# Kernel tuning notes

Hardware: AMD Instinct MI355X
Metric: run time of the kernel (lower is better)

Reference implementation:

```python
import jax, jax.numpy as jnp
import numpy as np

D = 768       # model dim
H = 12        # num heads
DH = 64       # hidden_dim per head (D == H*DH)
DT = 32       # time_dim
KTEMP = 1.0   # k_temperature
LN_EPS = 1e-5


def setup_inputs() -> dict:
    key = jax.random.key(0)
    ks = jax.random.split(key, 10)
    B, T = 2, 2048
    states = jax.random.normal(ks[0], (B, T, D), jnp.float32)
    attention_mask = jnp.ones((B, T), jnp.int32)
    s = 0.02
    Wq = jax.random.normal(ks[1], (H * DH, D), jnp.float32) * s
    Wk = jax.random.normal(ks[2], (H * DH, D), jnp.float32) * s
    bk = jax.random.normal(ks[3], (H * DH,), jnp.float32) * s
    Wv = jax.random.normal(ks[4], (H * DH, D), jnp.float32) * s
    bv = jnp.zeros((H * DH,), jnp.float32)           # V.bias zeroed in __init__
    Wo = jax.random.normal(ks[5], (D, H * DH), jnp.float32) * s
    bo = jnp.zeros((D,), jnp.float32)                # O.bias zeroed in __init__
    q_bias = jnp.zeros((H * DH,), jnp.float32)
    time_angle = jax.random.uniform(ks[6], (H, DT), jnp.float32) ** 10 + 1e-8
    head_time_delta = jax.random.uniform(ks[7], (H,), jnp.float32)
    ln_gamma = jnp.ones((D,), jnp.float32)
    ln_beta = jnp.zeros((D,), jnp.float32)
    return {"states": states, "attention_mask": attention_mask,
            "Wq": Wq, "Wk": Wk, "bk": bk, "Wv": Wv, "bv": bv,
            "Wo": Wo, "bo": bo, "q_bias": q_bias,
            "time_angle": time_angle, "head_time_delta": head_time_delta,
            "ln_gamma": ln_gamma, "ln_beta": ln_beta}


def reference(states, attention_mask, Wq, Wk, bk, Wv, bv, Wo, bo, q_bias,
              time_angle, head_time_delta, ln_gamma, ln_beta):
    B, T, _ = states.shape
    dtype = states.dtype
    mask = attention_mask.astype(dtype)[..., None, None]  # B T 1 1

    inv_sqrt_dh = 1.0 / np.sqrt(DH).astype(np.float32)

    def get_time(delta):
        # delta: [1,H,1] or scalar 0.0
        pos = jnp.arange(T, dtype=dtype)[:, None, None]     # T 1 1
        ang = (pos + delta) * time_angle[None]              # T H Dt
        c, s = jnp.cos(ang), jnp.sin(ang)
        return jnp.concatenate([c + s, c - s], axis=-1) * inv_sqrt_dh  # T H 2Dt

    # --- q path ---
    q = states @ Wq.T - jnp.exp(q_bias)                     # B T (H*Dh), Q has no bias
    q = jax.nn.sigmoid(q.reshape(B, T, H, DH)) / DH * mask  # B T H Dh
    time_q = get_time(head_time_delta[None, :, None])       # T H 2Dt (with delta)
    time_k = get_time(0.0)                                  # T H 2Dt
    q_timed = q.sum(-1, keepdims=True) * time_q             # B T H 2Dt
    # scores: B T(query) L(key) H -- the large materialized tensor
    scores = jnp.einsum('bthd,lhd->btlh', q_timed, time_k)

    # --- kv path ---
    k = (states @ Wk.T + bk).reshape(B, T, H, DH) / KTEMP * mask
    v = (states @ Wv.T + bv).reshape(B, T, H, DH)
    kv = jax.nn.softmax(k, axis=-1) * v                     # B T H Dh

    # --- aggregate ---
    loading = jnp.einsum('btlh,blhd->bthd', scores, kv).reshape(B, T, D)
    attn_out = loading @ Wo.T + bo

    # residual + layernorm (dropout is identity in eval)
    x = states + attn_out
    mu = x.mean(-1, keepdims=True)
    var = x.var(-1, keepdims=True)
    return (x - mu) * jax.lax.rsqrt(var + LN_EPS) * ln_gamma + ln_beta
```

## Files before the change

### kernel.cpp

```cpp
#include <hip/hip_runtime.h>
#include <math.h>
#include <stdint.h>

#define TT 2048
#define BB 2
#define DD 768
#define HH 12
#define DHH 64
#define DTT 32
#define NROW 4096

typedef float v4 __attribute__((ext_vector_type(4)));
typedef __attribute__((ext_vector_type(8))) short s8v;
typedef __attribute__((ext_vector_type(4))) float f4v;
typedef unsigned short u16;
typedef __attribute__((ext_vector_type(4))) unsigned short us4;

__device__ __forceinline__ u16 f2bf(float x) {
  unsigned u = __builtin_bit_cast(unsigned, x);
  u += 0x7fffu + ((u >> 16) & 1u);
  return (u16)(u >> 16);
}
__device__ __forceinline__ float bf2f(u16 b) {
  return __builtin_bit_cast(float, (unsigned)b << 16);
}
__device__ __forceinline__ float wave_sum(float v) {
#pragma unroll
  for (int m = 32; m > 0; m >>= 1) v += __shfl_xor(v, m, 64);
  return v;
}
__device__ __forceinline__ void gload16(const void* g, void* l) {
  __builtin_amdgcn_global_load_lds(
      (const __attribute__((address_space(1))) unsigned int*)g,
      (__attribute__((address_space(3))) unsigned int*)l, 16, 0, 0);
}
__device__ __forceinline__ void wait_vm3() {
  asm volatile("s_waitcnt vmcnt(3)" ::: "memory");
  __builtin_amdgcn_sched_barrier(0);
}
__device__ __forceinline__ void wait_vm0() {
  asm volatile("s_waitcnt vmcnt(0)" ::: "memory");
  __builtin_amdgcn_sched_barrier(0);
}
__device__ __forceinline__ void raw_barrier() {
  asm volatile("s_barrier" ::: "memory");
}

__global__ __launch_bounds__(256) void prep(
    const float* __restrict__ tang, const float* __restrict__ hdelta,
    const float* __restrict__ s, const float* __restrict__ wq,
    const float* __restrict__ wk, const float* __restrict__ wv,
    const float* __restrict__ wo, u16* __restrict__ timeqb,
    u16* __restrict__ timekb, u16* __restrict__ sb, u16* __restrict__ wqb,
    u16* __restrict__ wkvb, u16* __restrict__ wob) {
  int bid = blockIdx.x;
  if (bid < 3072) {
    int idx = bid * 256 + threadIdx.x;
    int d = idx % DTT;
    int h = (idx / DTT) % HH;
    int t = idx / (DTT * HH);
    float ang = tang[h * DTT + d];
    float sk, ck, sq, cq;
    sincosf((float)t * ang, &sk, &ck);
    sincosf(((float)t + hdelta[h]) * ang, &sq, &cq);
    timekb[t * DD + h * DHH + d]       = f2bf((ck + sk) * 0.125f);
    timekb[t * DD + h * DHH + d + DTT] = f2bf((ck - sk) * 0.125f);
    timeqb[t * DD + h * DHH + d]       = f2bf((cq + sq) * 0.125f);
    timeqb[t * DD + h * DHH + d + DTT] = f2bf((cq - sq) * 0.125f);
    return;
  }
  int idx = (bid - 3072) * 256 + threadIdx.x;
  int off = idx * 4;
  const float* src;
  u16* dst;
  int so, dof;
  if (off < 3145728) {
    src = s; dst = sb; so = off; dof = off;
  } else if (off < 3735552) {
    src = wq; dst = wqb; so = off - 3145728; dof = so;
  } else if (off < 4325376) {
    src = wk; so = off - 3735552;
    int j = so / 768, c = so - j * 768;
    int h = j >> 6, r = j & 63;
    dst = wkvb; dof = (h * 128 + r) * 768 + c;
  } else if (off < 4915200) {
    src = wv; so = off - 4325376;
    int j = so / 768, c = so - j * 768;
    int h = j >> 6, r = j & 63;
    dst = wkvb; dof = (h * 128 + 64 + r) * 768 + c;
  } else {
    src = wo; dst = wob; so = off - 4915200; dof = so;
  }
  v4 f = *(const v4*)&src[so];
  us4 o;
#pragma unroll
  for (int j = 0; j < 4; ++j) o[j] = f2bf(f[j]);
  *(us4*)&dst[dof] = o;
}

__global__ __launch_bounds__(256) void gemm_qkv_fused(
    const u16* __restrict__ A, const u16* __restrict__ Wqb,
    const u16* __restrict__ Wkvb, const float* __restrict__ qb,
    const float* __restrict__ bk, const float* __restrict__ bv,
    const int* __restrict__ amask, float* __restrict__ qsum,
    u16* __restrict__ kvb) {
  __shared__ __align__(16) u16 As[2][2176];
  __shared__ __align__(16) u16 Bs[2][4096];
  const int tid = threadIdx.x;
  const int l = tid & 63;
  const int w = tid >> 6;
  const int wr = w >> 1, wc = w & 1;
  const int bx = blockIdx.x;
  const bool isQ = bx < 6;
  const int i0 = blockIdx.y * 64;
  const u16* Bbase = isQ ? (Wqb + (size_t)bx * 128 * 768)
                         : (Wkvb + (size_t)(bx - 6) * 128 * 768);
  const int srow = tid >> 2, scol = (tid & 3) * 8;
  const u16* gA0 = A + (size_t)(i0 + srow) * 768 + scol;
  const u16* gB0 = Bbase + (size_t)srow * 768 + scol;
  const u16* gB1 = gB0 + (size_t)64 * 768;
  const int lo = tid * 8;
  f4v acc[2][4];
#pragma unroll
  for (int m = 0; m < 2; ++m)
#pragma unroll
    for (int n = 0; n < 4; ++n) acc[m][n] = (f4v){0.f, 0.f, 0.f, 0.f};

#define STAGE(kt, b)                       \
  do {                                     \
    int kb_ = (kt) << 5;                   \
    gload16(gA0 + kb_, &As[b][lo]);        \
    gload16(gB0 + kb_, &Bs[b][lo]);        \
    gload16(gB1 + kb_, &Bs[b][2048 + lo]); \
  } while (0)

  STAGE(0, 0);
  STAGE(1, 1);
  const int ar = wr * 32 + (l & 15);
  const int br = wc * 64 + (l & 15);
  const int kx = (l >> 4) * 8;
  int cb = 0;
  for (int kt = 0; kt < 24; ++kt) {
    if (kt < 23) wait_vm3();
    else wait_vm0();
    raw_barrier();
    s8v af[2], bf4[4];
#pragma unroll
    for (int m = 0; m < 2; ++m)
      af[m] = *(const s8v*)&As[cb][(ar + m * 16) * 32 + kx];
#pragma unroll
    for (int n = 0; n < 4; ++n)
      bf4[n] = *(const s8v*)&Bs[cb][(br + n * 16) * 32 + kx];
#pragma unroll
    for (int m = 0; m < 2; ++m)
#pragma unroll
      for (int n = 0; n < 4; ++n)
        acc[m][n] =
            __builtin_amdgcn_mfma_f32_16x16x32_bf16(af[m], bf4[n], acc[m][n], 0, 0, 0);
    raw_barrier();
    if (kt + 2 < 24) STAGE(kt + 2, cb);
    cb ^= 1;
  }
  __syncthreads();

  const int crow = i0 + wr * 32 + (l >> 4) * 4;
  if (isQ) {
    const int head = bx * 2 + wc;
    float eqb[4];
#pragma unroll
    for (int n = 0; n < 4; ++n)
      eqb[n] = expf(qb[head * 64 + n * 16 + (l & 15)]);
#pragma unroll
    for (int m = 0; m < 2; ++m)
#pragma unroll
      for (int r = 0; r < 4; ++r) {
        float ssum = 0.f;
#pragma unroll
        for (int n = 0; n < 4; ++n)
          ssum += 1.f / (1.f + expf(-(acc[m][n][r] - eqb[n])));
#pragma unroll
        for (int mm = 8; mm > 0; mm >>= 1) ssum += __shfl_xor(ssum, mm, 64);
        int row = crow + m * 16 + r;
        if ((l & 15) == 0)
          qsum[row * HH + head] = ssum * (float)amask[row] * (1.f / 64.f);
      }
  } else {
    const int head = bx - 6;
    u16* Ps = &As[0][0];
    if (wc == 0) {
#pragma unroll
      for (int m = 0; m < 2; ++m)
#pragma unroll
        for (int r = 0; r < 4; ++r) {
          int row = crow + m * 16 + r;
          float mk = (float)amask[row];
          float kv4[4];
#pragma unroll
          for (int n = 0; n < 4; ++n)
            kv4[n] = (acc[m][n][r] + bk[head * 64 + n * 16 + (l & 15)]) * mk;
          float mx = fmaxf(fmaxf(kv4[0], kv4[1]), fmaxf(kv4[2], kv4[3]));
#pragma unroll
          for (int mm = 8; mm > 0; mm >>= 1)
            mx = fmaxf(mx, __shfl_xor(mx, mm, 64));
          float e[4], es = 0.f;
#pragma unroll
          for (int n = 0; n < 4; ++n) { e[n] = expf(kv4[n] - mx); es += e[n]; }
#pragma unroll
          for (int mm = 8; mm > 0; mm >>= 1) es += __shfl_xor(es, mm, 64);
          float inv = 1.f / es;
          int lrow = wr * 32 + (l >> 4) * 4 + m * 16 + r;
#pragma unroll
          for (int n = 0; n < 4; ++n)
            Ps[lrow * 68 + n * 16 + (l & 15)] = f2bf(e[n] * inv);
        }
    }
    __syncthreads();
    if (wc == 1) {
#pragma unroll
      for (int m = 0; m < 2; ++m)
#pragma unroll
        for (int r = 0; r < 4; ++r) {
          int row = crow + m * 16 + r;
          int lrow = wr * 32 + (l >> 4) * 4 + m * 16 + r;
#pragma unroll
          for (int n = 0; n < 4; ++n) {
            int d = n * 16 + (l & 15);
            float p = bf2f(Ps[lrow * 68 + d]);
            float vv = acc[m][n][r] + bv[head * 64 + d];
            kvb[((size_t)row * HH + head) * 64 + d] = f2bf(p * vv);
          }
        }
    }
  }
}

__global__ __launch_bounds__(256) void calc_M(
    const u16* __restrict__ timekb, const u16* __restrict__ kvb,
    float* __restrict__ Mpart) {
  int blk = blockIdx.x;
  int split = blk & 15;
  int bh = blk >> 4;
  int b = bh / HH, h = bh % HH;
  __shared__ float Tk[64][68];
  __shared__ float Kv[64][68];
  int tid = threadIdx.x;
  int tx = tid & 15, ty = tid >> 4;
  float acc[4][4] = {};
  int t0 = split * 128;
  for (int tt = 0; tt < 128; tt += 64) {
#pragma unroll
    for (int p = 0; p < 4; ++p) {
      int f = tid + 256 * p;
      int r = f >> 4, c4 = (f & 15) << 2;
      int t = t0 + tt + r;
      us4 tk = *(const us4*)&timekb[(size_t)t * DD + h * DHH + c4];
      us4 kv = *(const us4*)&kvb[((size_t)(b * TT + t) * HH + h) * 64 + c4];
#pragma unroll
      for (int j = 0; j < 4; ++j) {
        Tk[r][c4 + j] = bf2f(tk[j]);
        Kv[r][c4 + j] = bf2f(kv[j]);
      }
    }
    __syncthreads();
#pragma unroll
    for (int kk = 0; kk < 64; ++kk) {
      v4 a = *(const v4*)&Tk[kk][ty * 4];
      v4 bv4 = *(const v4*)&Kv[kk][tx * 4];
#pragma unroll
      for (int r = 0; r < 4; ++r)
#pragma unroll
        for (int c = 0; c < 4; ++c) acc[r][c] += a[r] * bv4[c];
    }
    __syncthreads();
  }
#pragma unroll
  for (int r = 0; r < 4; ++r)
#pragma unroll
    for (int c = 0; c < 4; ++c)
      Mpart[(size_t)blk * 4096 + (tx * 4 + c) * 64 + (ty * 4 + r)] = acc[r][c];
}

__global__ __launch_bounds__(256) void reduce_M(
    const float* __restrict__ Mpart, u16* __restrict__ Mtb) {
  int idx = blockIdx.x * 256 + threadIdx.x;
  int bh = idx >> 12;
  int p = idx & 4095;
  float s = 0.f;
#pragma unroll
  for (int sp = 0; sp < 16; ++sp)
    s += Mpart[(size_t)((bh << 4) + sp) * 4096 + p];
  Mtb[(size_t)bh * 4096 + p] = f2bf(s);
}

__global__ __launch_bounds__(256) void calc_loading_mfma(
    const u16* __restrict__ timeqb, const u16* __restrict__ Mtb,
    const float* __restrict__ qsum, u16* __restrict__ loading) {
  const int bh = blockIdx.y;
  const int b = bh / HH, h = bh % HH;
  const int t0 = blockIdx.x * 128;
  __shared__ __align__(16) u16 Ms[64 * 72];
  for (int p = threadIdx.x; p < 4096; p += 256)
    Ms[(p >> 6) * 72 + (p & 63)] = Mtb[(size_t)bh * 4096 + p];
  __syncthreads();
  const int l = threadIdx.x & 63, w = threadIdx.x >> 6;
  f4v acc[2][4];
#pragma unroll
  for (int m = 0; m < 2; ++m)
#pragma unroll
    for (int n = 0; n < 4; ++n) acc[m][n] = (f4v){0.f, 0.f, 0.f, 0.f};
  const int arow = t0 + w * 32 + (l & 15);
  const int dcol = l & 15;
#pragma unroll
  for (int ks = 0; ks < 2; ++ks) {
    const int k0 = ks * 32 + (l >> 4) * 8;
    s8v af[2], bf4[4];
#pragma unroll
    for (int m = 0; m < 2; ++m)
      af[m] = *(const s8v*)&timeqb[(size_t)(arow + m * 16) * DD + h * DHH + k0];
#pragma unroll
    for (int n = 0; n < 4; ++n)
      bf4[n] = *(const s8v*)&Ms[(dcol + n * 16) * 72 + k0];
#pragma unroll
    for (int m = 0; m < 2; ++m)
#pragma unroll
      for (int n = 0; n < 4; ++n)
        acc[m][n] =
            __builtin_amdgcn_mfma_f32_16x16x32_bf16(af[m], bf4[n], acc[m][n], 0, 0, 0);
  }
  const int trow = t0 + w * 32 + (l >> 4) * 4;
  float qs[2][4];
#pragma unroll
  for (int m = 0; m < 2; ++m)
#pragma unroll
    for (int r = 0; r < 4; ++r)
      qs[m][r] = qsum[(b * TT + trow + m * 16 + r) * HH + h];
#pragma unroll
  for (int m = 0; m < 2; ++m)
#pragma unroll
    for (int n = 0; n < 4; ++n)
#pragma unroll
      for (int r = 0; r < 4; ++r) {
        int i = b * TT + trow + m * 16 + r;
        loading[(size_t)i * DD + h * DHH + n * 16 + (l & 15)] =
            f2bf(qs[m][r] * acc[m][n][r]);
      }
}

__global__ __launch_bounds__(256) void gemm_out(
    const u16* __restrict__ A, const u16* __restrict__ B, float* __restrict__ C,
    const float* __restrict__ bias, const float* __restrict__ res) {
  __shared__ __align__(16) u16 As[2][2176];
  __shared__ __align__(16) u16 Bs[2][4096];
  const int tid = threadIdx.x;
  const int l = tid & 63;
  const int w = tid >> 6;
  const int wr = w >> 1, wc = w & 1;
  const int i0 = blockIdx.y * 64, j0 = blockIdx.x * 128;
  const int srow = tid >> 2, scol = (tid & 3) * 8;
  const u16* gA0 = A + (size_t)(i0 + srow) * 768 + scol;
  const u16* gB0 = B + (size_t)(j0 + srow) * 768 + scol;
  const u16* gB1 = gB0 + (size_t)64 * 768;
  const int lo = tid * 8;
  f4v acc[2][4];
#pragma unroll
  for (int m = 0; m < 2; ++m)
#pragma unroll
    for (int n = 0; n < 4; ++n) acc[m][n] = (f4v){0.f, 0.f, 0.f, 0.f};
  STAGE(0, 0);
  STAGE(1, 1);
  const int ar = wr * 32 + (l & 15);
  const int br = wc * 64 + (l & 15);
  const int kx = (l >> 4) * 8;
  int cb = 0;
  for (int kt = 0; kt < 24; ++kt) {
    if (kt < 23) wait_vm3();
    else wait_vm0();
    raw_barrier();
    s8v af[2], bf4[4];
#pragma unroll
    for (int m = 0; m < 2; ++m)
      af[m] = *(const s8v*)&As[cb][(ar + m * 16) * 32 + kx];
#pragma unroll
    for (int n = 0; n < 4; ++n)
      bf4[n] = *(const s8v*)&Bs[cb][(br + n * 16) * 32 + kx];
#pragma unroll
    for (int m = 0; m < 2; ++m)
#pragma unroll
      for (int n = 0; n < 4; ++n)
        acc[m][n] =
            __builtin_amdgcn_mfma_f32_16x16x32_bf16(af[m], bf4[n], acc[m][n], 0, 0, 0);
    raw_barrier();
    if (kt + 2 < 24) STAGE(kt + 2, cb);
    cb ^= 1;
  }
  __syncthreads();
  const int crow = i0 + wr * 32 + (l >> 4) * 4;
  const int ccol = j0 + wc * 64 + (l & 15);
#pragma unroll
  for (int m = 0; m < 2; ++m)
#pragma unroll
    for (int n = 0; n < 4; ++n) {
      int col = ccol + n * 16;
      size_t base = (size_t)(crow + m * 16) * 768 + col;
#pragma unroll
      for (int r = 0; r < 4; ++r)
        C[base + (size_t)r * 768] =
            acc[m][n][r] + bias[col] + res[base + (size_t)r * 768];
    }
}

__global__ __launch_bounds__(256) void layernorm(
    const float* __restrict__ X, const float* __restrict__ gamma,
    const float* __restrict__ beta, float* __restrict__ out) {
  int i = blockIdx.x;
  const float* x = X + (size_t)i * 768;
  float vals[3];
  float s = 0.f, s2 = 0.f;
#pragma unroll
  for (int p = 0; p < 3; ++p) {
    float v = x[threadIdx.x + 256 * p];
    vals[p] = v;
    s += v;
    s2 += v * v;
  }
  s = wave_sum(s);
  s2 = wave_sum(s2);
  __shared__ float red[8];
  int w = threadIdx.x >> 6;
  if ((threadIdx.x & 63) == 0) {
    red[w] = s;
    red[4 + w] = s2;
  }
  __syncthreads();
  float stot = red[0] + red[1] + red[2] + red[3];
  float s2tot = red[4] + red[5] + red[6] + red[7];
  float mu = stot * (1.f / 768.f);
  float var = s2tot * (1.f / 768.f) - mu * mu;
  float rs = rsqrtf(var + 1e-5f);
#pragma unroll
  for (int p = 0; p < 3; ++p) {
    int j = threadIdx.x + 256 * p;
    out[(size_t)i * 768 + j] = (vals[p] - mu) * rs * gamma[j] + beta[j];
  }
}

extern "C" void kernel_launch(void* const* d_in, const int* in_sizes, int n_in,
                              void* d_out, int out_size, void* d_ws,
                              size_t ws_size, hipStream_t stream) {
  const float* states = (const float*)d_in[0];
  const int* amask    = (const int*)d_in[1];
  const float* Wq     = (const float*)d_in[2];
  const float* Wk     = (const float*)d_in[3];
  const float* bk     = (const float*)d_in[4];
  const float* Wv     = (const float*)d_in[5];
  const float* bv     = (const float*)d_in[6];
  const float* Wo     = (const float*)d_in[7];
  const float* bo     = (const float*)d_in[8];
  const float* qb     = (const float*)d_in[9];
  const float* tang   = (const float*)d_in[10];
  const float* hdelta = (const float*)d_in[11];
  const float* gamma  = (const float*)d_in[12];
  const float* beta   = (const float*)d_in[13];
  float* out = (float*)d_out;
  float* ws = (float*)d_ws;

  u16* timeqb = (u16*)(ws + 0);
  u16* timekb = (u16*)(ws + 786432);
  u16* Abf    = (u16*)(ws + 1572864);
  u16* Wqb    = (u16*)(ws + 3145728);
  u16* Wkvb   = (u16*)(ws + 3440640);
  u16* Wob    = (u16*)(ws + 4030464);
  float* qsum = ws + 4325376;
  u16* kvb    = (u16*)(ws + 4374528);
  float* Mpart= ws + 5160960;
  u16* Mtb    = (u16*)(ws + 6733824);
  u16* loadb  = (u16*)(ws + 6758400);
  float* xbuf = ws + 7544832;

  prep<<<8448, 256, 0, stream>>>(tang, hdelta, states, Wq, Wk, Wv, Wo, timeqb,
                                 timekb, Abf, Wqb, Wkvb, Wob);
  gemm_qkv_fused<<<dim3(18, 64), 256, 0, stream>>>(Abf, Wqb, Wkvb, qb, bk, bv,
                                                   amask, qsum, kvb);
  calc_M<<<384, 256, 0, stream>>>(timekb, kvb, Mpart);
  reduce_M<<<384, 256, 0, stream>>>(Mpart, Mtb);
  calc_loading_mfma<<<dim3(16, 24), 256, 0, stream>>>(timeqb, Mtb, qsum, loadb);
  gemm_out<<<dim3(6, 64), 256, 0, stream>>>(loadb, Wob, xbuf, bo, states);
  layernorm<<<4096, 256, 0, stream>>>(xbuf, gamma, beta, out);
}
```

Measured before the change: 93.76 us.

## Swizzle bf16 GEMM operands in global memory and use rotation recurrence for time tables

After: 91.83 us. -2.1%, faster.

```diff
diff --git a/kernel.cpp b/kernel.cpp
--- a/kernel.cpp
+++ b/kernel.cpp
@@ -44,6 +44,10 @@
 }
 __device__ __forceinline__ void raw_barrier() {
   asm volatile("s_barrier" ::: "memory");
+}
+__device__ __forceinline__ int swz_col(int row, int col) {
+  int ch = (col >> 3) & 3;
+  return (col & ~24) | (((ch ^ ((row >> 1) & 3)) & 3) << 3);
 }
 
 __global__ __launch_bounds__(256) void prep(
@@ -54,43 +58,57 @@
     u16* __restrict__ timekb, u16* __restrict__ sb, u16* __restrict__ wqb,
     u16* __restrict__ wkvb, u16* __restrict__ wob) {
   int bid = blockIdx.x;
-  if (bid < 3072) {
+  if (bid < 192) {
     int idx = bid * 256 + threadIdx.x;
-    int d = idx % DTT;
-    int h = (idx / DTT) % HH;
-    int t = idx / (DTT * HH);
+    int d = idx & 31;
+    int h = (idx >> 5) % HH;
+    int tc = idx / (32 * HH);
+    int t0 = tc * 16;
     float ang = tang[h * DTT + d];
-    float sk, ck, sq, cq;
-    sincosf((float)t * ang, &sk, &ck);
-    sincosf(((float)t + hdelta[h]) * ang, &sq, &cq);
-    timekb[t * DD + h * DHH + d]       = f2bf((ck + sk) * 0.125f);
-    timekb[t * DD + h * DHH + d + DTT] = f2bf((ck - sk) * 0.125f);
-    timeqb[t * DD + h * DHH + d]       = f2bf((cq + sq) * 0.125f);
-    timeqb[t * DD + h * DHH + d + DTT] = f2bf((cq - sq) * 0.125f);
+    float ca, sa;
+    sincosf(ang, &sa, &ca);
+    float ck, sk, cq, sq;
+    sincosf((float)t0 * ang, &sk, &ck);
+    sincosf(((float)t0 + hdelta[h]) * ang, &sq, &cq);
+#pragma unroll
+    for (int j = 0; j < 16; ++j) {
+      int t = t0 + j;
+      timekb[t * DD + h * DHH + d]       = f2bf((ck + sk) * 0.125f);
+      timekb[t * DD + h * DHH + d + DTT] = f2bf((ck - sk) * 0.125f);
+      timeqb[t * DD + h * DHH + d]       = f2bf((cq + sq) * 0.125f);
+      timeqb[t * DD + h * DHH + d + DTT] = f2bf((cq - sq) * 0.125f);
+      float ck2 = ck * ca - sk * sa;
+      sk = sk * ca + ck * sa;
+      ck = ck2;
+      float cq2 = cq * ca - sq * sa;
+      sq = sq * ca + cq * sa;
+      cq = cq2;
+    }
     return;
   }
-  int idx = (bid - 3072) * 256 + threadIdx.x;
+  int idx = (bid - 192) * 256 + threadIdx.x;
   int off = idx * 4;
   const float* src;
   u16* dst;
-  int so, dof;
+  int so, rr, cc;
   if (off < 3145728) {
-    src = s; dst = sb; so = off; dof = off;
+    src = s; dst = sb; so = off; rr = so / 768; cc = so % 768;
   } else if (off < 3735552) {
-    src = wq; dst = wqb; so = off - 3145728; dof = so;
+    src = wq; dst = wqb; so = off - 3145728; rr = so / 768; cc = so % 768;
   } else if (off < 4325376) {
     src = wk; so = off - 3735552;
-    int j = so / 768, c = so - j * 768;
+    int j = so / 768; cc = so - j * 768;
     int h = j >> 6, r = j & 63;
-    dst = wkvb; dof = (h * 128 + r) * 768 + c;
+    dst = wkvb; rr = h * 128 + r;
   } else if (off < 4915200) {
     src = wv; so = off - 4325376;
-    int j = so / 768, c = so - j * 768;
+    int j = so / 768; cc = so - j * 768;
     int h = j >> 6, r = j & 63;
-    dst = wkvb; dof = (h * 128 + 64 + r) * 768 + c;
+    dst = wkvb; rr = h * 128 + 64 + r;
   } else {
-    src = wo; dst = wob; so = off - 4915200; dof = so;
-  }
+    src = wo; dst = wob; so = off - 4915200; rr = so / 768; cc = so % 768;
+  }
+  int dof = rr * 768 + swz_col(rr, cc);
   v4 f = *(const v4*)&src[so];
   us4 o;
 #pragma unroll
@@ -136,9 +154,17 @@
 
   STAGE(0, 0);
   STAGE(1, 1);
-  const int ar = wr * 32 + (l & 15);
-  const int br = wc * 64 + (l & 15);
-  const int kx = (l >> 4) * 8;
+  int aoff[2], boff[4];
+#pragma unroll
+  for (int m = 0; m < 2; ++m) {
+    int row = wr * 32 + (l & 15) + m * 16;
+    aoff[m] = row * 32 + (((l >> 4) ^ ((row >> 1) & 3)) << 3);
+  }
+#pragma unroll
+  for (int n = 0; n < 4; ++n) {
+    int row = wc * 64 + (l & 15) + n * 16;
+    boff[n] = row * 32 + (((l >> 4) ^ ((row >> 1) & 3)) << 3);
+  }
   int cb = 0;
   for (int kt = 0; kt < 24; ++kt) {
     if (kt < 23) wait_vm3();
@@ -146,11 +172,9 @@
     raw_barrier();
     s8v af[2], bf4[4];
 #pragma unroll
-    for (int m = 0; m < 2; ++m)
-      af[m] = *(const s8v*)&As[cb][(ar + m * 16) * 32 + kx];
-#pragma unroll
-    for (int n = 0; n < 4; ++n)
-      bf4[n] = *(const s8v*)&Bs[cb][(br + n * 16) * 32 + kx];
+    for (int m = 0; m < 2; ++m) af[m] = *(const s8v*)&As[cb][aoff[m]];
+#pragma unroll
+    for (int n = 0; n < 4; ++n) bf4[n] = *(const s8v*)&Bs[cb][boff[n]];
 #pragma unroll
     for (int m = 0; m < 2; ++m)
 #pragma unroll
@@ -341,7 +365,8 @@
 #pragma unroll
       for (int r = 0; r < 4; ++r) {
         int i = b * TT + trow + m * 16 + r;
-        loading[(size_t)i * DD + h * DHH + n * 16 + (l & 15)] =
+        int col = h * DHH + n * 16 + (l & 15);
+        loading[(size_t)i * DD + swz_col(i, col)] =
             f2bf(qs[m][r] * acc[m][n][r]);
       }
 }
@@ -368,9 +393,17 @@
     for (int n = 0; n < 4; ++n) acc[m][n] = (f4v){0.f, 0.f, 0.f, 0.f};
   STAGE(0, 0);
   STAGE(1, 1);
-  const int ar = wr * 32 + (l & 15);
-  const int br = wc * 64 + (l & 15);
-  const int kx = (l >> 4) * 8;
+  int aoff[2], boff[4];
+#pragma unroll
+  for (int m = 0; m < 2; ++m) {
+    int row = wr * 32 + (l & 15) + m * 16;
+    aoff[m] = row * 32 + (((l >> 4) ^ ((row >> 1) & 3)) << 3);
+  }
+#pragma unroll
+  for (int n = 0; n < 4; ++n) {
+    int row = wc * 64 + (l & 15) + n * 16;
+    boff[n] = row * 32 + (((l >> 4) ^ ((row >> 1) & 3)) << 3);
+  }
   int cb = 0;
   for (int kt = 0; kt < 24; ++kt) {
     if (kt < 23) wait_vm3();
@@ -378,11 +411,9 @@
     raw_barrier();
     s8v af[2], bf4[4];
 #pragma unroll
-    for (int m = 0; m < 2; ++m)
-      af[m] = *(const s8v*)&As[cb][(ar + m * 16) * 32 + kx];
-#pragma unroll
-    for (int n = 0; n < 4; ++n)
-      bf4[n] = *(const s8v*)&Bs[cb][(br + n * 16) * 32 + kx];
+    for (int m = 0; m < 2; ++m) af[m] = *(const s8v*)&As[cb][aoff[m]];
+#pragma unroll
+    for (int n = 0; n < 4; ++n) bf4[n] = *(const s8v*)&Bs[cb][boff[n]];
 #pragma unroll
     for (int m = 0; m < 2; ++m)
 #pragma unroll
@@ -477,7 +508,7 @@
   u16* loadb  = (u16*)(ws + 6758400);
   float* xbuf = ws + 7544832;
 
-  prep<<<8448, 256, 0, stream>>>(tang, hdelta, states, Wq, Wk, Wv, Wo, timeqb,
+  prep<<<5568, 256, 0, stream>>>(tang, hdelta, states, Wq, Wk, Wv, Wo, timeqb,
                                  timekb, Abf, Wqb, Wkvb, Wob);
   gemm_qkv_fused<<<dim3(18, 64), 256, 0, stream>>>(Abf, Wqb, Wkvb, qb, bk, bv,
                                                    amask, qsum, kvb);
```
